# Kernel optimization log

Measured on AMD Instinct MI355X. Metric: run time of the kernel, lower is better.

## Reference

```python
import jax, jax.numpy as jnp
import numpy as np

B, S, H = 4, 1024, 1024
NH = 16
DH = H // NH  # 64


def setup_inputs() -> dict:
    key = jax.random.key(0)
    ks = jax.random.split(key, 8)
    std = 1.0 / np.sqrt(H)
    return {
        "query": jax.random.normal(ks[0], (B, S, H), jnp.float32),
        "key": jax.random.normal(ks[1], (B, S, H), jnp.float32),
        "value": jax.random.normal(ks[2], (B, S, H), jnp.float32),
        "masks": jnp.ones((B, S), jnp.float32),
        "Wq": jax.random.normal(ks[3], (H, H), jnp.float32) * std,
        "bq": jnp.zeros((H,), jnp.float32),
        "Wk": jax.random.normal(ks[4], (H, H), jnp.float32) * std,
        "bk": jnp.zeros((H,), jnp.float32),
        "Wv": jax.random.normal(ks[5], (H, H), jnp.float32) * std,
        "bv": jnp.zeros((H,), jnp.float32),
    }


def reference(query, key, value, masks, Wq, bq, Wk, bk, Wv, bv):
    # ReLU-gated projections (torch Linear: x @ W.T + b)
    qp = jax.nn.relu(jnp.einsum("bsh,oh->bso", query, Wq) + bq)
    kp = jax.nn.relu(jnp.einsum("bsh,oh->bso", key, Wk) + bk)
    vp = jax.nn.relu(jnp.einsum("bsh,oh->bso", value, Wv) + bv)
    # chunk(dim=2)+cat(dim=0) == split hidden into (NH, DH) contiguous slices
    qh = qp.reshape(B, S, NH, DH)
    kh = kp.reshape(B, S, NH, DH)
    vh = vp.reshape(B, S, NH, DH)
    scale = 1.0 / jnp.sqrt(jnp.asarray(DH, qp.dtype))
    # [B, NH, Sq, Sk]
    alpha = jnp.einsum("bqnd,bknd->bnqk", qh, kh) * scale
    alpha = jax.nn.softmax(alpha, axis=-1)
    # post-softmax multiplicative mask, applied per QUERY position
    alpha = alpha * masks[:, None, :, None]
    hiddens = jnp.einsum("bnqk,bknd->bqnd", alpha, vh).reshape(B, S, H)
    return hiddens + query
```

## Files before the change

### kernel.cpp

```cpp
#include <hip/hip_runtime.h>


typedef __attribute__((ext_vector_type(8))) __bf16 bf16x8;
typedef __attribute__((ext_vector_type(4))) float f32x4;
typedef __attribute__((ext_vector_type(16))) float f32x16;
typedef __attribute__((ext_vector_type(8))) unsigned short u16x8;
typedef __attribute__((ext_vector_type(4))) unsigned short u16x4;

#define XQ_OFF 0u
#define XK_OFF 4194304u
#define XV_OFF 8388608u
#define WQ_OFF 12582912u
#define WK_OFF 13631488u
#define WV_OFF 14680064u
#define QP_OFF 15728640u
#define KP_OFF 19922944u
#define VT_OFF 24117248u

__device__ __forceinline__ unsigned short f2bf(float f) {
  union { float f; unsigned int u; } c; c.f = f;
  return (unsigned short)((c.u + 0x7fffu + ((c.u >> 16) & 1u)) >> 16);
}

__global__ __launch_bounds__(256) void cvt_kernel(
    const float* __restrict__ q, const float* __restrict__ k, const float* __restrict__ v,
    const float* __restrict__ wq, const float* __restrict__ wk, const float* __restrict__ wv,
    unsigned short* __restrict__ ws) {
  const int z = blockIdx.y;
  const float* src; unsigned short* dst; int n;
  switch (z) {
    case 0: src = q;  dst = ws + XQ_OFF; n = 4194304; break;
    case 1: src = k;  dst = ws + XK_OFF; n = 4194304; break;
    case 2: src = v;  dst = ws + XV_OFF; n = 4194304; break;
    case 3: src = wq; dst = ws + WQ_OFF; n = 1048576; break;
    case 4: src = wk; dst = ws + WK_OFF; n = 1048576; break;
    default: src = wv; dst = ws + WV_OFF; n = 1048576; break;
  }
  const int i8 = (blockIdx.x * 256 + threadIdx.x) * 8;
  if (i8 >= n) return;
  const float4 f0 = *(const float4*)(src + i8);
  const float4 f1 = *(const float4*)(src + i8 + 4);
  u16x8 r;
  r[0] = f2bf(f0.x); r[1] = f2bf(f0.y); r[2] = f2bf(f0.z); r[3] = f2bf(f0.w);
  r[4] = f2bf(f1.x); r[5] = f2bf(f1.y); r[6] = f2bf(f1.z); r[7] = f2bf(f1.w);
  *(u16x8*)(dst + i8) = r;
}

__global__ __launch_bounds__(256) void proj_gemm(
    unsigned short* __restrict__ ws,
    const float* __restrict__ bq, const float* __restrict__ bk, const float* __restrict__ bv) {
  __shared__ unsigned short smem[32768];
  const int z = blockIdx.z;
  const unsigned short* X = ws + (z == 0 ? XQ_OFF : z == 1 ? XK_OFF : XV_OFF);
  const unsigned short* W = ws + (z == 0 ? WQ_OFF : z == 1 ? WK_OFF : WV_OFF);
  unsigned short* P = ws + (z == 0 ? QP_OFF : z == 1 ? KP_OFF : VT_OFF);
  const float* bias = z == 0 ? bq : z == 1 ? bk : bv;

  const int tid  = threadIdx.x;
  const int lane = tid & 63;
  const int w    = tid >> 6;
  const int l31  = lane & 31;
  const int g    = lane >> 5;
  const int wr = w >> 1, wc = w & 1;

  const int lin = blockIdx.x + 8 * blockIdx.y;
  const int xcd = lin & 7;
  const int idx = lin >> 3;
  const int m0 = (xcd * 4 + (idx >> 3)) * 128;
  const int n0 = (idx & 7) * 128;

  f32x16 acc[2][2];
#pragma unroll
  for (int i = 0; i < 2; ++i)
#pragma unroll
    for (int j = 0; j < 2; ++j)
#pragma unroll
      for (int r = 0; r < 16; ++r) acc[i][j][r] = 0.f;

  const int c1 = 256 + tid;
  const int row0 = tid >> 2, kc0 = (((tid & 3) ^ ((row0 >> 1) & 3)) * 8);
  const int row1 = c1 >> 2,  kc1 = (((c1 & 3) ^ ((row1 >> 1) & 3)) * 8);
  const unsigned short* gA0 = X + (size_t)(m0 + row0) * 1024 + kc0;
  const unsigned short* gA1 = X + (size_t)(m0 + row1) * 1024 + kc1;
  const unsigned short* gB0 = W + (size_t)(n0 + row0) * 1024 + kc0;
  const unsigned short* gB1 = W + (size_t)(n0 + row1) * 1024 + kc1;
  const int d0 = w * 512, d1 = 2048 + w * 512;

  auto stage = [&](int buf) {
    unsigned short* Ab = smem + buf * 8192;
    unsigned short* Bb = Ab + 4096;
    __builtin_amdgcn_global_load_lds((const __attribute__((address_space(1))) void*)gA0,
                                     (__attribute__((address_space(3))) void*)(Ab + d0), 16, 0, 0);
    __builtin_amdgcn_global_load_lds((const __attribute__((address_space(1))) void*)gB0,
                                     (__attribute__((address_space(3))) void*)(Bb + d0), 16, 0, 0);
    __builtin_amdgcn_global_load_lds((const __attribute__((address_space(1))) void*)gA1,
                                     (__attribute__((address_space(3))) void*)(Ab + d1), 16, 0, 0);
    __builtin_amdgcn_global_load_lds((const __attribute__((address_space(1))) void*)gB1,
                                     (__attribute__((address_space(3))) void*)(Bb + d1), 16, 0, 0);
    gA0 += 32; gA1 += 32; gB0 += 32; gB1 += 32;
  };
  auto compute = [&](int buf) {
    const unsigned short* Ab = smem + buf * 8192;
    const unsigned short* Bb = Ab + 4096;
    bf16x8 af[2][2], bfv[2][2];
#pragma unroll
    for (int mt = 0; mt < 2; ++mt)
#pragma unroll
      for (int kk = 0; kk < 2; ++kk) {
        const int ra = wr * 64 + mt * 32 + l31;
        af[mt][kk] = *(const bf16x8*)&Ab[ra * 32 + (((kk * 2 + g) ^ ((ra >> 1) & 3)) * 8)];
      }
#pragma unroll
    for (int nt = 0; nt < 2; ++nt)
#pragma unroll
      for (int kk = 0; kk < 2; ++kk) {
        const int rb = wc * 64 + nt * 32 + l31;
        bfv[nt][kk] = *(const bf16x8*)&Bb[rb * 32 + (((kk * 2 + g) ^ ((rb >> 1) & 3)) * 8)];
      }
    __builtin_amdgcn_s_setprio(1);
#pragma unroll
    for (int mt = 0; mt < 2; ++mt)
#pragma unroll
      for (int nt = 0; nt < 2; ++nt)
#pragma unroll
        for (int kk = 0; kk < 2; ++kk)
          acc[mt][nt] = __builtin_amdgcn_mfma_f32_32x32x16_bf16(af[mt][kk], bfv[nt][kk],
                                                                acc[mt][nt], 0, 0, 0);
    __builtin_amdgcn_s_setprio(0);
  };

  stage(0); stage(1); stage(2);
  for (int t = 0; t < 29; ++t) {
    asm volatile("s_waitcnt vmcnt(8)" ::: "memory");
    __builtin_amdgcn_s_barrier();
    stage((t + 3) & 3);
    compute(t & 3);
  }
  asm volatile("s_waitcnt vmcnt(8)" ::: "memory");
  __builtin_amdgcn_s_barrier();
  compute(1);
  asm volatile("s_waitcnt vmcnt(4)" ::: "memory");
  __builtin_amdgcn_s_barrier();
  compute(2);
  asm volatile("s_waitcnt vmcnt(0)" ::: "memory");
  __builtin_amdgcn_s_barrier();
  compute(3);

  unsigned short* Tw = smem + w * 4608;
  if (z != 2) {
#pragma unroll
    for (int mt = 0; mt < 2; ++mt)
#pragma unroll
      for (int nt = 0; nt < 2; ++nt) {
        const float bvv = bias[n0 + wc * 64 + nt * 32 + l31];
#pragma unroll
        for (int reg = 0; reg < 16; ++reg) {
          const int rloc = (reg & 3) + 8 * (reg >> 2) + 4 * g;
          float v = acc[mt][nt][reg] + bvv;
          v = v > 0.f ? v : 0.f;
          Tw[(mt * 32 + rloc) * 72 + nt * 32 + l31] = f2bf(v);
        }
      }
    const int row0g = m0 + wr * 64;
    const int colb  = n0 + wc * 64;
#pragma unroll
    for (int i = 0; i < 8; ++i) {
      const int rr = i * 8 + (lane >> 3);
      const int cc = (lane & 7) * 8;
      *(u16x8*)&P[(size_t)(row0g + rr) * 1024 + colb + cc] = *(const u16x8*)&Tw[rr * 72 + cc];
    }
  } else {
#pragma unroll
    for (int mt = 0; mt < 2; ++mt)
#pragma unroll
      for (int nt = 0; nt < 2; ++nt) {
        const float bvv = bias[n0 + wc * 64 + nt * 32 + l31];
#pragma unroll
        for (int rq = 0; rq < 4; ++rq) {
          u16x4 pk;
#pragma unroll
          for (int r = 0; r < 4; ++r) {
            float v = acc[mt][nt][rq * 4 + r] + bvv;
            v = v > 0.f ? v : 0.f;
            pk[r] = f2bf(v);
          }
          *(u16x4*)&Tw[(nt * 32 + l31) * 72 + mt * 32 + rq * 8 + g * 4] = pk;
        }
      }
    const int h2 = (n0 >> 6) + wc;
    const int bb = m0 >> 10;
    const int s0 = (m0 & 1023) + wr * 64;
#pragma unroll
    for (int i = 0; i < 8; ++i) {
      const int rr = i * 8 + (lane >> 3);
      const int cc = (lane & 7) * 8;
      *(u16x8*)&P[((size_t)(bb * 16 + h2) * 64 + rr) * 1024 + s0 + cc] =
          *(const u16x8*)&Tw[rr * 72 + cc];
    }
  }
}

__global__ __launch_bounds__(256) void attn_kernel(
    const unsigned short* __restrict__ QP, const unsigned short* __restrict__ KP,
    const unsigned short* __restrict__ VT, const float* __restrict__ masks,
    const float* __restrict__ query, float* __restrict__ out) {
  __shared__ unsigned short Kt[2][64 * 64];
  __shared__ unsigned short Vt[2][64 * 64];
  __shared__ unsigned short Pl[4][32 * 72];
  const int tid  = threadIdx.x;
  const int lane = tid & 63;
  const int w    = tid >> 6;
  const int quad = lane >> 4;
  const int l15  = lane & 15;
  const int bh = blockIdx.x;
  const int b = bh >> 4, h = bh & 15;
  const int q0w = blockIdx.y * 128 + w * 32;
  const size_t base = (size_t)b * 1024 * 1024;

  bf16x8 qf[2][2];
#pragma unroll
  for (int mt = 0; mt < 2; ++mt)
#pragma unroll
    for (int kk = 0; kk < 2; ++kk)
      qf[mt][kk] = *(const bf16x8*)&QP[base + (size_t)(q0w + mt * 16 + l15) * 1024 +
                                       h * 64 + kk * 32 + quad * 8];

  f32x4 o[2][4];
  float lsum[2] = {0.f, 0.f};
#pragma unroll
  for (int mt = 0; mt < 2; ++mt)
#pragma unroll
    for (int nd = 0; nd < 4; ++nd) o[mt][nd] = f32x4{0.f, 0.f, 0.f, 0.f};

  const int r_st = lane >> 3;
  const int pc   = lane & 7;
  const int swz  = l15 & 7;
  const float cvt = 0.18033688011112042f;

  auto stage = [&](int key0, int buf) {
#pragma unroll
    for (int t = 0; t < 2; ++t) {
      const int rowk = (w * 2 + t) * 8 + r_st;
      const int lc   = pc ^ (rowk & 7);
      const unsigned short* gk = &KP[base + (size_t)(key0 + rowk) * 1024 + h * 64 + lc * 8];
      const unsigned short* gv = &VT[((size_t)bh * 64 + rowk) * 1024 + key0 + lc * 8];
      __builtin_amdgcn_global_load_lds((const __attribute__((address_space(1))) void*)gk,
                                       (__attribute__((address_space(3))) void*)&Kt[buf][(w * 2 + t) * 512],
                                       16, 0, 0);
      __builtin_amdgcn_global_load_lds((const __attribute__((address_space(1))) void*)gv,
                                       (__attribute__((address_space(3))) void*)&Vt[buf][(w * 2 + t) * 512],
                                       16, 0, 0);
    }
  };

  stage(0, 0);
  for (int kb = 0; kb < 16; ++kb) {
    __syncthreads();
    if (kb < 15) stage((kb + 1) * 64, (kb + 1) & 1);
    const unsigned short* Ktb = Kt[kb & 1];
    const unsigned short* Vtb = Vt[kb & 1];

    bf16x8 kf[2][4];
#pragma unroll
    for (int kk = 0; kk < 2; ++kk)
#pragma unroll
      for (int ni = 0; ni < 4; ++ni)
        kf[kk][ni] = *(const bf16x8*)&Ktb[(ni * 16 + l15) * 64 + ((kk * 4 + quad) ^ swz) * 8];

#pragma unroll
    for (int mt = 0; mt < 2; ++mt) {
      f32x4 st[4];
#pragma unroll
      for (int ni = 0; ni < 4; ++ni) st[ni] = f32x4{0.f, 0.f, 0.f, 0.f};
#pragma unroll
      for (int kk = 0; kk < 2; ++kk)
#pragma unroll
        for (int ni = 0; ni < 4; ++ni)
          st[ni] = __builtin_amdgcn_mfma_f32_16x16x32_bf16(kf[kk][ni], qf[mt][kk], st[ni], 0, 0, 0);
      float ls = 0.f;
#pragma unroll
      for (int ni = 0; ni < 4; ++ni) {
        float p0 = exp2f(fmaf(st[ni][0], cvt, -8.0f));
        float p1 = exp2f(fmaf(st[ni][1], cvt, -8.0f));
        float p2 = exp2f(fmaf(st[ni][2], cvt, -8.0f));
        float p3 = exp2f(fmaf(st[ni][3], cvt, -8.0f));
        ls += (p0 + p1) + (p2 + p3);
        const unsigned int u0 = __float_as_uint(p0) + 0x8000u;
        const unsigned int u1 = __float_as_uint(p1) + 0x8000u;
        const unsigned int u2 = __float_as_uint(p2) + 0x8000u;
        const unsigned int u3 = __float_as_uint(p3) + 0x8000u;
        uint2 pk;
        pk.x = (u0 >> 16) | (u1 & 0xffff0000u);
        pk.y = (u2 >> 16) | (u3 & 0xffff0000u);
        *(uint2*)&Pl[w][(mt * 16 + l15) * 72 + ni * 16 + quad * 4] = pk;
      }
      lsum[mt] += ls;
    }

#pragma unroll
    for (int kk = 0; kk < 2; ++kk) {
      bf16x8 pa[2];
#pragma unroll
      for (int mt = 0; mt < 2; ++mt)
        pa[mt] = *(const bf16x8*)&Pl[w][(mt * 16 + l15) * 72 + kk * 32 + quad * 8];
#pragma unroll
      for (int nd = 0; nd < 4; ++nd) {
        bf16x8 vf = *(const bf16x8*)&Vtb[(nd * 16 + l15) * 64 + ((kk * 4 + quad) ^ swz) * 8];
#pragma unroll
        for (int mt = 0; mt < 2; ++mt)
          o[mt][nd] = __builtin_amdgcn_mfma_f32_16x16x32_bf16(pa[mt], vf, o[mt][nd], 0, 0, 0);
      }
    }
  }

#pragma unroll
  for (int mt = 0; mt < 2; ++mt) {
    lsum[mt] += __shfl_xor(lsum[mt], 16);
    lsum[mt] += __shfl_xor(lsum[mt], 32);
  }

#pragma unroll
  for (int mt = 0; mt < 2; ++mt)
#pragma unroll
    for (int r = 0; r < 4; ++r) {
      const int rq = quad * 4 + r;
      const float ls = __shfl(lsum[mt], (lane & 48) | rq);
      const int row = q0w + mt * 16 + rq;
      const float scale = masks[b * 1024 + row] / ls;
#pragma unroll
      for (int nd = 0; nd < 4; ++nd) {
        const int col = h * 64 + nd * 16 + l15;
        const size_t gi = base + (size_t)row * 1024 + col;
        out[gi] = o[mt][nd][r] * scale + query[gi];
      }
    }
}

extern "C" void kernel_launch(void* const* d_in, const int* in_sizes, int n_in,
                              void* d_out, int out_size, void* d_ws, size_t ws_size,
                              hipStream_t stream) {
  const float* q     = (const float*)d_in[0];
  const float* k     = (const float*)d_in[1];
  const float* v     = (const float*)d_in[2];
  const float* masks = (const float*)d_in[3];
  const float* Wq    = (const float*)d_in[4];
  const float* bq    = (const float*)d_in[5];
  const float* Wk    = (const float*)d_in[6];
  const float* bk    = (const float*)d_in[7];
  const float* Wv    = (const float*)d_in[8];
  const float* bv    = (const float*)d_in[9];
  float* out = (float*)d_out;
  unsigned short* ws = (unsigned short*)d_ws;

  cvt_kernel<<<dim3(2048, 6), 256, 0, stream>>>(q, k, v, Wq, Wk, Wv, ws);
  proj_gemm<<<dim3(8, 32, 3), 256, 0, stream>>>(ws, bq, bk, bv);
  attn_kernel<<<dim3(64, 8), 256, 0, stream>>>(ws + QP_OFF, ws + KP_OFF, ws + VT_OFF,
                                               masks, q, out);
}
```

Baseline: 184.9 us.

## Load K/V fragments directly from global into registers, compute row sums via MFMA

Removes the shared-memory double buffers for K and V and the per-iteration block barrier. Each wave now loads its K and V MFMA fragments straight from global memory into registers, with K software-prefetched one block ahead in a ping-pong register pair. The softmax row sums are now accumulated by an extra MFMA against a vector of ones, replacing the scalar adds and final shuffles, and launch bounds request two blocks per SM. The cost is that each wave re-reads K/V from global/L2 instead of sharing it through LDS, and register pressure rises.

```diff
diff --git a/kernel.cpp b/kernel.cpp
--- a/kernel.cpp
+++ b/kernel.cpp
@@ -200,12 +200,10 @@
   }
 }
 
-__global__ __launch_bounds__(256) void attn_kernel(
+__global__ __launch_bounds__(256, 2) void attn_kernel(
     const unsigned short* __restrict__ QP, const unsigned short* __restrict__ KP,
     const unsigned short* __restrict__ VT, const float* __restrict__ masks,
     const float* __restrict__ query, float* __restrict__ out) {
-  __shared__ unsigned short Kt[2][64 * 64];
-  __shared__ unsigned short Vt[2][64 * 64];
   __shared__ unsigned short Pl[4][32 * 72];
   const int tid  = threadIdx.x;
   const int lane = tid & 63;
@@ -226,46 +224,39 @@
                                        h * 64 + kk * 32 + quad * 8];
 
   f32x4 o[2][4];
-  float lsum[2] = {0.f, 0.f};
-#pragma unroll
-  for (int mt = 0; mt < 2; ++mt)
+  f32x4 lacc[2];
+#pragma unroll
+  for (int mt = 0; mt < 2; ++mt) {
+    lacc[mt] = f32x4{0.f, 0.f, 0.f, 0.f};
 #pragma unroll
     for (int nd = 0; nd < 4; ++nd) o[mt][nd] = f32x4{0.f, 0.f, 0.f, 0.f};
-
-  const int r_st = lane >> 3;
-  const int pc   = lane & 7;
-  const int swz  = l15 & 7;
+  }
+
+  bf16x8 onesb;
+#pragma unroll
+  for (int i = 0; i < 8; ++i) onesb[i] = (__bf16)1.0f;
+
   const float cvt = 0.18033688011112042f;
 
-  auto stage = [&](int key0, int buf) {
-#pragma unroll
-    for (int t = 0; t < 2; ++t) {
-      const int rowk = (w * 2 + t) * 8 + r_st;
-      const int lc   = pc ^ (rowk & 7);
-      const unsigned short* gk = &KP[base + (size_t)(key0 + rowk) * 1024 + h * 64 + lc * 8];
-      const unsigned short* gv = &VT[((size_t)bh * 64 + rowk) * 1024 + key0 + lc * 8];
-      __builtin_amdgcn_global_load_lds((const __attribute__((address_space(1))) void*)gk,
-                                       (__attribute__((address_space(3))) void*)&Kt[buf][(w * 2 + t) * 512],
-                                       16, 0, 0);
-      __builtin_amdgcn_global_load_lds((const __attribute__((address_space(1))) void*)gv,
-                                       (__attribute__((address_space(3))) void*)&Vt[buf][(w * 2 + t) * 512],
-                                       16, 0, 0);
-    }
+  const unsigned short* Kbase = KP + base + (size_t)l15 * 1024 + h * 64 + quad * 8;
+  const unsigned short* Vbase = VT + ((size_t)bh * 64 + l15) * 1024 + quad * 8;
+
+  auto loadK = [&](bf16x8 (&kf)[2][4], int kb) {
+#pragma unroll
+    for (int kk = 0; kk < 2; ++kk)
+#pragma unroll
+      for (int ni = 0; ni < 4; ++ni)
+        kf[kk][ni] = *(const bf16x8*)(Kbase + (size_t)(kb * 64 + ni * 16) * 1024 + kk * 32);
   };
 
-  stage(0, 0);
-  for (int kb = 0; kb < 16; ++kb) {
-    __syncthreads();
-    if (kb < 15) stage((kb + 1) * 64, (kb + 1) & 1);
-    const unsigned short* Ktb = Kt[kb & 1];
-    const unsigned short* Vtb = Vt[kb & 1];
-
-    bf16x8 kf[2][4];
+  auto step = [&](int kb, bf16x8 (&kC)[2][4], bf16x8 (&kN)[2][4]) {
+    bf16x8 vfr[2][4];
 #pragma unroll
     for (int kk = 0; kk < 2; ++kk)
 #pragma unroll
-      for (int ni = 0; ni < 4; ++ni)
-        kf[kk][ni] = *(const bf16x8*)&Ktb[(ni * 16 + l15) * 64 + ((kk * 4 + quad) ^ swz) * 8];
+      for (int nd = 0; nd < 4; ++nd)
+        vfr[kk][nd] = *(const bf16x8*)(Vbase + (size_t)nd * 16384 + kb * 64 + kk * 32);
+    if (kb < 15) loadK(kN, kb + 1);
 
 #pragma unroll
     for (int mt = 0; mt < 2; ++mt) {
@@ -276,15 +267,13 @@
       for (int kk = 0; kk < 2; ++kk)
 #pragma unroll
         for (int ni = 0; ni < 4; ++ni)
-          st[ni] = __builtin_amdgcn_mfma_f32_16x16x32_bf16(kf[kk][ni], qf[mt][kk], st[ni], 0, 0, 0);
-      float ls = 0.f;
+          st[ni] = __builtin_amdgcn_mfma_f32_16x16x32_bf16(kC[kk][ni], qf[mt][kk], st[ni], 0, 0, 0);
 #pragma unroll
       for (int ni = 0; ni < 4; ++ni) {
         float p0 = exp2f(fmaf(st[ni][0], cvt, -8.0f));
         float p1 = exp2f(fmaf(st[ni][1], cvt, -8.0f));
         float p2 = exp2f(fmaf(st[ni][2], cvt, -8.0f));
         float p3 = exp2f(fmaf(st[ni][3], cvt, -8.0f));
-        ls += (p0 + p1) + (p2 + p3);
         const unsigned int u0 = __float_as_uint(p0) + 0x8000u;
         const unsigned int u1 = __float_as_uint(p1) + 0x8000u;
         const unsigned int u2 = __float_as_uint(p2) + 0x8000u;
@@ -294,7 +283,6 @@
         pk.y = (u2 >> 16) | (u3 & 0xffff0000u);
         *(uint2*)&Pl[w][(mt * 16 + l15) * 72 + ni * 16 + quad * 4] = pk;
       }
-      lsum[mt] += ls;
     }
 
 #pragma unroll
@@ -304,19 +292,22 @@
       for (int mt = 0; mt < 2; ++mt)
         pa[mt] = *(const bf16x8*)&Pl[w][(mt * 16 + l15) * 72 + kk * 32 + quad * 8];
 #pragma unroll
-      for (int nd = 0; nd < 4; ++nd) {
-        bf16x8 vf = *(const bf16x8*)&Vtb[(nd * 16 + l15) * 64 + ((kk * 4 + quad) ^ swz) * 8];
+      for (int mt = 0; mt < 2; ++mt)
+        lacc[mt] = __builtin_amdgcn_mfma_f32_16x16x32_bf16(pa[mt], onesb, lacc[mt], 0, 0, 0);
+#pragma unroll
+      for (int nd = 0; nd < 4; ++nd)
 #pragma unroll
         for (int mt = 0; mt < 2; ++mt)
-          o[mt][nd] = __builtin_amdgcn_mfma_f32_16x16x32_bf16(pa[mt], vf, o[mt][nd], 0, 0, 0);
-      }
-    }
-  }
-
-#pragma unroll
-  for (int mt = 0; mt < 2; ++mt) {
-    lsum[mt] += __shfl_xor(lsum[mt], 16);
-    lsum[mt] += __shfl_xor(lsum[mt], 32);
+          o[mt][nd] = __builtin_amdgcn_mfma_f32_16x16x32_bf16(pa[mt], vfr[kk][nd], o[mt][nd], 0, 0, 0);
+    }
+  };
+
+  bf16x8 kA[2][4], kB[2][4];
+  loadK(kA, 0);
+#pragma unroll 1
+  for (int kb2 = 0; kb2 < 8; ++kb2) {
+    step(kb2 * 2,     kA, kB);
+    step(kb2 * 2 + 1, kB, kA);
   }
 
 #pragma unroll
@@ -324,9 +315,8 @@
 #pragma unroll
     for (int r = 0; r < 4; ++r) {
       const int rq = quad * 4 + r;
-      const float ls = __shfl(lsum[mt], (lane & 48) | rq);
       const int row = q0w + mt * 16 + rq;
-      const float scale = masks[b * 1024 + row] / ls;
+      const float scale = masks[b * 1024 + row] / lacc[mt][r];
 #pragma unroll
       for (int nd = 0; nd < 4; ++nd) {
         const int col = h * 64 + nd * 16 + l15;
```

After: 210.5 us. +13.8%, slower.

## Triple-buffer attention K/V staging and compute row sums via MFMA

Applied to the files above, without the earlier changes.

Moves the attention kernel's K/V LDS staging from double to triple buffering with explicit vmcnt waits and raw barriers, so each load has two iterations to complete. It computes softmax row sums with an extra MFMA against a ones vector on the bf16-rounded probabilities, which removes the scalar adds and cross-lane shuffles. It also adds s_setprio around the MFMA blocks, uses the raw exp2 builtin, and sets launch_bounds occupancy to 2. The cost is more LDS per block and row sums taken from rounded bf16 values instead of fp32.

```diff
diff --git a/kernel.cpp b/kernel.cpp
--- a/kernel.cpp
+++ b/kernel.cpp
@@ -200,12 +200,12 @@
   }
 }
 
-__global__ __launch_bounds__(256) void attn_kernel(
+__global__ __launch_bounds__(256, 2) void attn_kernel(
     const unsigned short* __restrict__ QP, const unsigned short* __restrict__ KP,
     const unsigned short* __restrict__ VT, const float* __restrict__ masks,
     const float* __restrict__ query, float* __restrict__ out) {
-  __shared__ unsigned short Kt[2][64 * 64];
-  __shared__ unsigned short Vt[2][64 * 64];
+  __shared__ unsigned short Kt[3][64 * 64];
+  __shared__ unsigned short Vt[3][64 * 64];
   __shared__ unsigned short Pl[4][32 * 72];
   const int tid  = threadIdx.x;
   const int lane = tid & 63;
@@ -226,11 +226,17 @@
                                        h * 64 + kk * 32 + quad * 8];
 
   f32x4 o[2][4];
-  float lsum[2] = {0.f, 0.f};
-#pragma unroll
-  for (int mt = 0; mt < 2; ++mt)
+  f32x4 lacc[2];
+#pragma unroll
+  for (int mt = 0; mt < 2; ++mt) {
+    lacc[mt] = f32x4{0.f, 0.f, 0.f, 0.f};
 #pragma unroll
     for (int nd = 0; nd < 4; ++nd) o[mt][nd] = f32x4{0.f, 0.f, 0.f, 0.f};
+  }
+
+  bf16x8 onesb;
+#pragma unroll
+  for (int i = 0; i < 8; ++i) onesb[i] = (__bf16)1.0f;
 
   const int r_st = lane >> 3;
   const int pc   = lane & 7;
@@ -253,12 +259,9 @@
     }
   };
 
-  stage(0, 0);
-  for (int kb = 0; kb < 16; ++kb) {
-    __syncthreads();
-    if (kb < 15) stage((kb + 1) * 64, (kb + 1) & 1);
-    const unsigned short* Ktb = Kt[kb & 1];
-    const unsigned short* Vtb = Vt[kb & 1];
+  auto step = [&](int buf) {
+    const unsigned short* Ktb = Kt[buf];
+    const unsigned short* Vtb = Vt[buf];
 
     bf16x8 kf[2][4];
 #pragma unroll
@@ -272,19 +275,19 @@
       f32x4 st[4];
 #pragma unroll
       for (int ni = 0; ni < 4; ++ni) st[ni] = f32x4{0.f, 0.f, 0.f, 0.f};
+      __builtin_amdgcn_s_setprio(1);
 #pragma unroll
       for (int kk = 0; kk < 2; ++kk)
 #pragma unroll
         for (int ni = 0; ni < 4; ++ni)
           st[ni] = __builtin_amdgcn_mfma_f32_16x16x32_bf16(kf[kk][ni], qf[mt][kk], st[ni], 0, 0, 0);
-      float ls = 0.f;
+      __builtin_amdgcn_s_setprio(0);
 #pragma unroll
       for (int ni = 0; ni < 4; ++ni) {
-        float p0 = exp2f(fmaf(st[ni][0], cvt, -8.0f));
-        float p1 = exp2f(fmaf(st[ni][1], cvt, -8.0f));
-        float p2 = exp2f(fmaf(st[ni][2], cvt, -8.0f));
-        float p3 = exp2f(fmaf(st[ni][3], cvt, -8.0f));
-        ls += (p0 + p1) + (p2 + p3);
+        float p0 = __builtin_amdgcn_exp2f(fmaf(st[ni][0], cvt, -8.0f));
+        float p1 = __builtin_amdgcn_exp2f(fmaf(st[ni][1], cvt, -8.0f));
+        float p2 = __builtin_amdgcn_exp2f(fmaf(st[ni][2], cvt, -8.0f));
+        float p3 = __builtin_amdgcn_exp2f(fmaf(st[ni][3], cvt, -8.0f));
         const unsigned int u0 = __float_as_uint(p0) + 0x8000u;
         const unsigned int u1 = __float_as_uint(p1) + 0x8000u;
         const unsigned int u2 = __float_as_uint(p2) + 0x8000u;
@@ -294,7 +297,6 @@
         pk.y = (u2 >> 16) | (u3 & 0xffff0000u);
         *(uint2*)&Pl[w][(mt * 16 + l15) * 72 + ni * 16 + quad * 4] = pk;
       }
-      lsum[mt] += ls;
     }
 
 #pragma unroll
@@ -303,6 +305,10 @@
 #pragma unroll
       for (int mt = 0; mt < 2; ++mt)
         pa[mt] = *(const bf16x8*)&Pl[w][(mt * 16 + l15) * 72 + kk * 32 + quad * 8];
+      __builtin_amdgcn_s_setprio(1);
+#pragma unroll
+      for (int mt = 0; mt < 2; ++mt)
+        lacc[mt] = __builtin_amdgcn_mfma_f32_16x16x32_bf16(pa[mt], onesb, lacc[mt], 0, 0, 0);
 #pragma unroll
       for (int nd = 0; nd < 4; ++nd) {
         bf16x8 vf = *(const bf16x8*)&Vtb[(nd * 16 + l15) * 64 + ((kk * 4 + quad) ^ swz) * 8];
@@ -310,23 +316,29 @@
         for (int mt = 0; mt < 2; ++mt)
           o[mt][nd] = __builtin_amdgcn_mfma_f32_16x16x32_bf16(pa[mt], vf, o[mt][nd], 0, 0, 0);
       }
-    }
-  }
-
-#pragma unroll
-  for (int mt = 0; mt < 2; ++mt) {
-    lsum[mt] += __shfl_xor(lsum[mt], 16);
-    lsum[mt] += __shfl_xor(lsum[mt], 32);
-  }
+      __builtin_amdgcn_s_setprio(0);
+    }
+  };
+
+  stage(0, 0);
+  stage(64, 1);
+  for (int kb = 0; kb < 15; ++kb) {
+    asm volatile("s_waitcnt vmcnt(4)" ::: "memory");
+    __builtin_amdgcn_s_barrier();
+    if (kb < 14) stage((kb + 2) * 64, (kb + 2) % 3);
+    step(kb % 3);
+  }
+  asm volatile("s_waitcnt vmcnt(0)" ::: "memory");
+  __builtin_amdgcn_s_barrier();
+  step(0);
 
 #pragma unroll
   for (int mt = 0; mt < 2; ++mt)
 #pragma unroll
     for (int r = 0; r < 4; ++r) {
       const int rq = quad * 4 + r;
-      const float ls = __shfl(lsum[mt], (lane & 48) | rq);
       const int row = q0w + mt * 16 + rq;
-      const float scale = masks[b * 1024 + row] / ls;
+      const float scale = masks[b * 1024 + row] / lacc[mt][r];
 #pragma unroll
       for (int nd = 0; nd < 4; ++nd) {
         const int col = h * 64 + nd * 16 + l15;
```

Result: faster. 173.6 us (-6.2%).
